# Kernel tuning notes

Measured on AMD Instinct MI355X. Metric: run time of the kernel, lower is better.

The kernel has to match this reference:

```python
import jax, jax.numpy as jnp
import numpy as np


def setup_inputs() -> dict:
    key = jax.random.key(0)
    ks = jax.random.split(key, 12)
    B, T, N, H = 32, 128, 256, 512
    s = 0.05
    return {
        "data": jax.random.normal(ks[0], (B, T, N), jnp.float32),
        "h0": jax.random.normal(ks[1], (B, H), jnp.float32),
        "gru_kernel": jax.random.normal(ks[2], (N, 3 * H), jnp.float32) * s,
        "gru_rkernel": jax.random.normal(ks[3], (H, 3 * H), jnp.float32) * s,
        "gru_bias": jax.random.normal(ks[4], (2, 3 * H), jnp.float32) * s,  # (input_bias, recurrent_bias), reset_after=True
        "w1_w": jax.random.normal(ks[5], (T, T), jnp.float32) * s,
        "w1_b": jax.random.normal(ks[6], (T,), jnp.float32) * s,
        "w2_w": jax.random.normal(ks[7], (H, T), jnp.float32) * s,
        "w2_b": jax.random.normal(ks[8], (T,), jnp.float32) * s,
        "v_w": jax.random.normal(ks[9], (T, 1), jnp.float32) * s,
        "v_b": jax.random.normal(ks[10], (1,), jnp.float32) * s,
        "n": N,
    }


def reference(data, h0, gru_kernel, gru_rkernel, gru_bias, w1_w, w1_b, w2_w, w2_b, v_w, v_b, n):
    B, T, N = data.shape
    b_in, b_rec = gru_bias[0], gru_bias[1]

    # Keras GRUCell (reset_after=True, gate order z,r,h)
    def step(h, x_t):
        mx = x_t @ gru_kernel + b_in          # (B,3H)
        mh = h @ gru_rkernel + b_rec          # (B,3H)
        xz, xr, xh = jnp.split(mx, 3, axis=-1)
        hz, hr, hh = jnp.split(mh, 3, axis=-1)
        z = jax.nn.sigmoid(xz + hz)
        r = jax.nn.sigmoid(xr + hr)
        c = jnp.tanh(xh + r * hh)
        h_new = z * h + (1.0 - z) * c
        return h_new, h_new

    xs = jnp.swapaxes(data, 0, 1)                               # (T,B,N)
    _, hs = jax.lax.scan(step, h0, xs)                          # (T,B,H) hidden state after each step

    # Input attention, vectorized over t (attention does not feed back into the GRU)
    x_perm = jnp.swapaxes(data, 1, 2)                           # (B,N,T)
    score_x = jnp.einsum('bnt,tu->bnu', x_perm, w1_w) + w1_b    # (B,N,T), constant across steps
    h_proj = hs @ w2_w + w2_b                                   # (T,B,T)
    e = jnp.tanh(score_x[None, :, :, :] + h_proj[:, :, None, :])  # (T,B,N,T)
    score = jnp.einsum('tbnu,u->tbn', e, v_w[:, 0]) + v_b[0]    # (T,B,N)
    alpha = jax.nn.softmax(score, axis=-1)                      # (T,B,N) softmax over features

    # Replicates tf.reshape(alpha_seq.stack(), (-1, T, n)) on (T,B,1,N) (row-major)
    alpha_seq = alpha.reshape(-1, T, N)                         # (B,T,N) via flat reindex, as in original
    return data * alpha_seq
```

## Files before the change

kernel.cpp:

```cpp
#include <hip/hip_runtime.h>
#include <math.h>

#define BB 32
#define TT 128
#define NF 256
#define HH 512
#define G3 1536
#define NWG 64

__device__ __forceinline__ float sigmoidf_(float x) { return 1.f / (1.f + __expf(-x)); }
__device__ __forceinline__ float tanh_fast(float x) {
    float e = __expf(2.f * x);
    return 1.f - 2.f / (e + 1.f);
}
__device__ __forceinline__ float sel4_(float a0, float a1, float a2, float a3, int s) {
    float s01 = (s & 1) ? a1 : a0;
    float s23 = (s & 1) ? a3 : a2;
    return (s & 2) ? s23 : s01;
}

__global__ __launch_bounds__(256) void k_hinit(const float* __restrict__ h0,
                                               float* __restrict__ hg2) {
    int idx = blockIdx.x * 256 + threadIdx.x;
    int i = idx & 511, b = idx >> 9;
    hg2[i * BB + b] = h0[b * HH + i];
}

__global__ __launch_bounds__(256) void k_pack(const float* __restrict__ rk,
                                              float4* __restrict__ rk4) {
    int gidx = blockIdx.x * 256 + threadIdx.x;
    int wg = gidx >> 12;
    int idx = gidx & 4095;
    int k = idx >> 3, s = idx & 7;
    int jjL = s ^ (((k >> 7) & 3) << 1);
    const float* r = rk + (size_t)k * G3 + wg * 8 + jjL;
    rk4[gidx] = make_float4(r[0], r[512], r[1024], 0.f);
}

__global__ __launch_bounds__(256) void k_mx(const float* __restrict__ data,
                                            const float* __restrict__ gk,
                                            const float* __restrict__ bias_in,
                                            float* __restrict__ mxT) {
    __shared__ __align__(16) float xs[NF * 8];
    int bx = blockIdx.x;
    int t = bx >> 2, b0 = (bx & 3) * 8;
    int tid = threadIdx.x;
    for (int idx = tid; idx < 8 * NF; idx += 256) {
        int bb = idx >> 8, k = idx & 255;
        xs[k * 8 + bb] = data[((size_t)(b0 + bb) * TT + t) * NF + k];
    }
    __syncthreads();
    float acc[6][8];
#pragma unroll
    for (int jj = 0; jj < 6; jj++)
#pragma unroll
        for (int bb = 0; bb < 8; bb++) acc[jj][bb] = 0.f;

    for (int k = 0; k < NF; k++) {
        float4 xa = *(const float4*)&xs[k * 8];
        float4 xb = *(const float4*)&xs[k * 8 + 4];
        float xv[8] = {xa.x, xa.y, xa.z, xa.w, xb.x, xb.y, xb.z, xb.w};
#pragma unroll
        for (int jj = 0; jj < 6; jj++) {
            float g = gk[(size_t)k * G3 + jj * 256 + tid];
#pragma unroll
            for (int bb = 0; bb < 8; bb++) acc[jj][bb] += g * xv[bb];
        }
    }
#pragma unroll
    for (int jj = 0; jj < 6; jj++) {
        int j = jj * 256 + tid;
        float bi = bias_in[j];
#pragma unroll
        for (int bb = 0; bb < 8; bb++)
            mxT[((size_t)t * G3 + j) * BB + b0 + bb] = acc[jj][bb] + bi;
    }
}

extern __shared__ float4 wl4_dyn[];

__global__ __launch_bounds__(256, 1) void k_gstep(const float4* __restrict__ rk4,
                                                  const float* __restrict__ gbias,
                                                  const float* __restrict__ mxT,
                                                  float* __restrict__ hg2,
                                                  float* __restrict__ hs,
                                                  int t) {
    __shared__ __align__(16) float4 h4[HH * 8];
    const int tid = threadIdx.x;
    const int wg  = blockIdx.x;
    const int jj  = tid >> 5;
    const int bq  = (tid >> 2) & 7;
    const int ks  = tid & 3;
    const int i0  = wg * 8;
    const int i   = i0 + jj;
    const int batch = bq * 4 + ks;
    const int jjs = jj ^ (ks << 1);
    const int bqs = bq ^ (ks << 1);

    {
        const float4* src = rk4 + (size_t)wg * 4096;
#pragma unroll
        for (int it = 0; it < 16; it++) {
            int idx = it * 256 + tid;
            wl4_dyn[idx] = src[idx];
        }
    }
    {
        const float4* hgr = (const float4*)(hg2 + (t & 1) * (HH * BB));
#pragma unroll
        for (int it = 0; it < 16; it++) {
            int idx = it * 256 + tid;
            h4[idx] = hgr[idx ^ ((((idx >> 10) & 3)) << 1)];
        }
    }
    const float* brec = gbias + G3;
    const float bz = brec[i], br_ = brec[512 + i], bh = brec[1024 + i];
    __syncthreads();

    const float* mxc = mxT + (size_t)t * G3 * BB;
    float mz = mxc[(size_t)i * BB + batch];
    float mr = mxc[(size_t)(512 + i) * BB + batch];
    float mh = mxc[(size_t)(1024 + i) * BB + batch];

    float az0 = 0.f, az1 = 0.f, az2 = 0.f, az3 = 0.f;
    float ar0 = 0.f, ar1 = 0.f, ar2 = 0.f, ar3 = 0.f;
    float ah0 = 0.f, ah1 = 0.f, ah2 = 0.f, ah3 = 0.f;
    const float4* wp  = wl4_dyn + ks * 1024 + jjs;
    const float4* hp2 = &h4[ks * 1024 + bqs];
#pragma unroll 4
    for (int kk = 0; kk < 128; kk++) {
        float4 w = wp[kk * 8];
        float4 h = hp2[kk * 8];
        az0 += w.x * h.x; az1 += w.x * h.y; az2 += w.x * h.z; az3 += w.x * h.w;
        ar0 += w.y * h.x; ar1 += w.y * h.y; ar2 += w.y * h.z; ar3 += w.y * h.w;
        ah0 += w.z * h.x; ah1 += w.z * h.y; ah2 += w.z * h.z; ah3 += w.z * h.w;
    }

    az0 += __shfl_xor(az0, 1); az1 += __shfl_xor(az1, 1);
    az2 += __shfl_xor(az2, 1); az3 += __shfl_xor(az3, 1);
    ar0 += __shfl_xor(ar0, 1); ar1 += __shfl_xor(ar1, 1);
    ar2 += __shfl_xor(ar2, 1); ar3 += __shfl_xor(ar3, 1);
    ah0 += __shfl_xor(ah0, 1); ah1 += __shfl_xor(ah1, 1);
    ah2 += __shfl_xor(ah2, 1); ah3 += __shfl_xor(ah3, 1);
    az0 += __shfl_xor(az0, 2); az1 += __shfl_xor(az1, 2);
    az2 += __shfl_xor(az2, 2); az3 += __shfl_xor(az3, 2);
    ar0 += __shfl_xor(ar0, 2); ar1 += __shfl_xor(ar1, 2);
    ar2 += __shfl_xor(ar2, 2); ar3 += __shfl_xor(ar3, 2);
    ah0 += __shfl_xor(ah0, 2); ah1 += __shfl_xor(ah1, 2);
    ah2 += __shfl_xor(ah2, 2); ah3 += __shfl_xor(ah3, 2);

    float azt = sel4_(az0, az1, az2, az3, ks);
    float art = sel4_(ar0, ar1, ar2, ar3, ks);
    float aht = sel4_(ah0, ah1, ah2, ah3, ks);

    float z = sigmoidf_(mz + azt + bz);
    float r = sigmoidf_(mr + art + br_);
    float c = tanhf(mh + r * (aht + bh));
    float hold = ((const float*)&h4[i * 8 + (bq ^ ((((i >> 7) & 3)) << 1))])[ks];
    float hn = z * hold + (1.f - z) * c;

    hg2[((t + 1) & 1) * (HH * BB) + i * BB + batch] = hn;

    __syncthreads();
    float* hstage = (float*)wl4_dyn;
    hstage[jj * 36 + batch] = hn;
    __syncthreads();
    {
        int b2 = tid >> 3, ii = tid & 7;
        hs[((size_t)t * BB + b2) * HH + i0 + ii] = hstage[ii * 36 + b2];
    }
}

__global__ __launch_bounds__(256) void k_sx(const float* __restrict__ data,
                                            const float* __restrict__ w1,
                                            const float* __restrict__ w1b,
                                            float* __restrict__ sx) {
    int bx = blockIdx.x;
    int b = bx >> 4, ug = bx & 15;
    int n = threadIdx.x;
    float acc[8] = {0, 0, 0, 0, 0, 0, 0, 0};
    const float* dp = data + (size_t)b * TT * NF + n;
    for (int t = 0; t < TT; t++) {
        float x = dp[(size_t)t * NF];
#pragma unroll
        for (int uu = 0; uu < 8; uu++) acc[uu] += x * w1[t * TT + ug * 8 + uu];
    }
#pragma unroll
    for (int uu = 0; uu < 8; uu++) {
        int u = ug * 8 + uu;
        sx[((size_t)b * TT + u) * NF + n] = acc[uu] + w1b[u];
    }
}

__global__ __launch_bounds__(256) void k_hp(const float* __restrict__ hs,
                                            const float* __restrict__ w2,
                                            const float* __restrict__ w2b,
                                            float* __restrict__ hp) {
    __shared__ float hsl[8 * HH];
    int r0 = blockIdx.x * 8;
    int tid = threadIdx.x;
    for (int idx = tid; idx < 8 * HH; idx += 256)
        hsl[idx] = hs[(size_t)r0 * HH + idx];
    __syncthreads();
    int u = tid & 127, rh = tid >> 7;
    float acc[4] = {0, 0, 0, 0};
    for (int k = 0; k < HH; k++) {
        float w = w2[k * TT + u];
#pragma unroll
        for (int rr = 0; rr < 4; rr++) acc[rr] += hsl[(rh * 4 + rr) * HH + k] * w;
    }
    float wb = w2b[u];
#pragma unroll
    for (int rr = 0; rr < 4; rr++)
        hp[(size_t)(r0 + rh * 4 + rr) * TT + u] = acc[rr] + wb;
}

__global__ __launch_bounds__(256) void k_attn(const float* __restrict__ data,
                                              const float* __restrict__ sx,
                                              const float* __restrict__ hp,
                                              const float* __restrict__ v_w,
                                              const float* __restrict__ v_b,
                                              float* __restrict__ out) {
    __shared__ float hv[TT];
    __shared__ float vv[TT];
    __shared__ float red[8];
    int r = blockIdx.x;
    int b = r & 31;
    int n = threadIdx.x;
    if (n < TT) {
        hv[n] = hp[(size_t)r * TT + n];
        vv[n] = v_w[n];
    }
    __syncthreads();
    float s = v_b[0];
    const float* sxp = sx + (size_t)b * TT * NF + n;
    for (int u = 0; u < TT; u++) {
        float e = tanh_fast(sxp[(size_t)u * NF] + hv[u]);
        s += vv[u] * e;
    }
    float m = s;
#pragma unroll
    for (int off = 32; off >= 1; off >>= 1) m = fmaxf(m, __shfl_xor(m, off));
    int lane = n & 63, wid = n >> 6;
    if (lane == 0) red[wid] = m;
    __syncthreads();
    float bm = fmaxf(fmaxf(red[0], red[1]), fmaxf(red[2], red[3]));
    float p = __expf(s - bm);
    float ps = p;
#pragma unroll
    for (int off = 32; off >= 1; off >>= 1) ps += __shfl_xor(ps, off);
    if (lane == 0) red[4 + wid] = ps;
    __syncthreads();
    float denom = red[4] + red[5] + red[6] + red[7];
    float alpha = p / denom;
    size_t idx = (size_t)r * NF + n;
    out[idx] = data[idx] * alpha;
}

extern "C" void kernel_launch(void* const* d_in, const int* in_sizes, int n_in,
                              void* d_out, int out_size, void* d_ws, size_t ws_size,
                              hipStream_t stream) {
    const float* data = (const float*)d_in[0];
    const float* h0   = (const float*)d_in[1];
    const float* gk   = (const float*)d_in[2];
    const float* rk   = (const float*)d_in[3];
    const float* gb   = (const float*)d_in[4];
    const float* w1   = (const float*)d_in[5];
    const float* w1b  = (const float*)d_in[6];
    const float* w2   = (const float*)d_in[7];
    const float* w2b  = (const float*)d_in[8];
    const float* vw   = (const float*)d_in[9];
    const float* vb   = (const float*)d_in[10];
    float* out = (float*)d_out;

    float* ws  = (float*)d_ws;
    float* mxT = ws;
    float* hs  = mxT + 6291456;
    float* sxb = hs + 2097152;
    float* hpb = sxb + 1048576;
    float* hg2 = hpb + 524288;
    float4* rk4 = (float4*)(hg2 + 32768);

    k_hinit<<<64, 256, 0, stream>>>(h0, hg2);
    k_pack<<<1024, 256, 0, stream>>>(rk, rk4);
    k_mx<<<512, 256, 0, stream>>>(data, gk, gb, mxT);

    for (int t = 0; t < TT; t++)
        k_gstep<<<NWG, 256, 65536, stream>>>(rk4, gb, mxT, hg2, hs, t);

    k_sx<<<512, 256, 0, stream>>>(data, w1, w1b, sxb);
    k_hp<<<512, 256, 0, stream>>>(hs, w2, w2b, hpb);
    k_attn<<<4096, 256, 0, stream>>>(data, sxb, hpb, vw, vb, out);
}
```

Baseline: 1.278 ms.

## Use direct global-to-LDS loads, merge init kernels, split k_mx wider

The per-step GRU kernel now stages recurrent weights and hidden state into shared memory with global_load_lds intrinsics, so the copies no longer pass through registers. The h-init and weight-pack kernels are merged into one launch, and k_mx is split three ways over gate columns to raise its workgroup count. tanh uses a hardware reciprocal and the attention loop is unrolled. Risks: the async LDS loads must complete before the barrier, and the fast reciprocal changes precision slightly.

After: 1.176 ms. 8.0% less time.

```diff
diff --git a/kernel.cpp b/kernel.cpp
--- a/kernel.cpp
+++ b/kernel.cpp
@@ -11,7 +11,7 @@
 __device__ __forceinline__ float sigmoidf_(float x) { return 1.f / (1.f + __expf(-x)); }
 __device__ __forceinline__ float tanh_fast(float x) {
     float e = __expf(2.f * x);
-    return 1.f - 2.f / (e + 1.f);
+    return 1.f - 2.f * __builtin_amdgcn_rcpf(e + 1.f);
 }
 __device__ __forceinline__ float sel4_(float a0, float a1, float a2, float a3, int s) {
     float s01 = (s & 1) ? a1 : a0;
@@ -19,22 +19,24 @@
     return (s & 2) ? s23 : s01;
 }
 
-__global__ __launch_bounds__(256) void k_hinit(const float* __restrict__ h0,
-                                               float* __restrict__ hg2) {
-    int idx = blockIdx.x * 256 + threadIdx.x;
-    int i = idx & 511, b = idx >> 9;
-    hg2[i * BB + b] = h0[b * HH + i];
-}
-
-__global__ __launch_bounds__(256) void k_pack(const float* __restrict__ rk,
-                                              float4* __restrict__ rk4) {
-    int gidx = blockIdx.x * 256 + threadIdx.x;
-    int wg = gidx >> 12;
-    int idx = gidx & 4095;
-    int k = idx >> 3, s = idx & 7;
-    int jjL = s ^ (((k >> 7) & 3) << 1);
-    const float* r = rk + (size_t)k * G3 + wg * 8 + jjL;
-    rk4[gidx] = make_float4(r[0], r[512], r[1024], 0.f);
+__global__ __launch_bounds__(256) void k_packinit(const float* __restrict__ rk,
+                                                  float4* __restrict__ rk4,
+                                                  const float* __restrict__ h0,
+                                                  float* __restrict__ hg2) {
+    int bid = blockIdx.x;
+    if (bid < 1024) {
+        int gidx = bid * 256 + threadIdx.x;
+        int wg = gidx >> 12;
+        int idx = gidx & 4095;
+        int k = idx >> 3, s = idx & 7;
+        int jjL = s ^ (((k >> 7) & 3) << 1);
+        const float* r = rk + (size_t)k * G3 + wg * 8 + jjL;
+        rk4[gidx] = make_float4(r[0], r[512], r[1024], 0.f);
+    } else {
+        int idx = (bid - 1024) * 256 + threadIdx.x;
+        int i = idx & 511, b = idx >> 9;
+        hg2[i * BB + b] = h0[b * HH + i];
+    }
 }
 
 __global__ __launch_bounds__(256) void k_mx(const float* __restrict__ data,
@@ -43,33 +45,38 @@
                                             float* __restrict__ mxT) {
     __shared__ __align__(16) float xs[NF * 8];
     int bx = blockIdx.x;
-    int t = bx >> 2, b0 = (bx & 3) * 8;
+    int t = bx / 12;
+    int rem = bx - t * 12;
+    int bg = rem / 3;
+    int jth = rem - bg * 3;
+    int b0 = bg * 8;
     int tid = threadIdx.x;
     for (int idx = tid; idx < 8 * NF; idx += 256) {
         int bb = idx >> 8, k = idx & 255;
         xs[k * 8 + bb] = data[((size_t)(b0 + bb) * TT + t) * NF + k];
     }
     __syncthreads();
-    float acc[6][8];
-#pragma unroll
-    for (int jj = 0; jj < 6; jj++)
+    float acc[2][8];
+#pragma unroll
+    for (int jj = 0; jj < 2; jj++)
 #pragma unroll
         for (int bb = 0; bb < 8; bb++) acc[jj][bb] = 0.f;
 
+    const float* gkc = gk + jth * 512 + tid;
     for (int k = 0; k < NF; k++) {
         float4 xa = *(const float4*)&xs[k * 8];
         float4 xb = *(const float4*)&xs[k * 8 + 4];
         float xv[8] = {xa.x, xa.y, xa.z, xa.w, xb.x, xb.y, xb.z, xb.w};
 #pragma unroll
-        for (int jj = 0; jj < 6; jj++) {
-            float g = gk[(size_t)k * G3 + jj * 256 + tid];
+        for (int jj = 0; jj < 2; jj++) {
+            float g = gkc[(size_t)k * G3 + jj * 256];
 #pragma unroll
             for (int bb = 0; bb < 8; bb++) acc[jj][bb] += g * xv[bb];
         }
     }
 #pragma unroll
-    for (int jj = 0; jj < 6; jj++) {
-        int j = jj * 256 + tid;
+    for (int jj = 0; jj < 2; jj++) {
+        int j = jth * 512 + jj * 256 + tid;
         float bi = bias_in[j];
 #pragma unroll
         for (int bb = 0; bb < 8; bb++)
@@ -102,7 +109,9 @@
 #pragma unroll
         for (int it = 0; it < 16; it++) {
             int idx = it * 256 + tid;
-            wl4_dyn[idx] = src[idx];
+            __builtin_amdgcn_global_load_lds(
+                (const __attribute__((address_space(1))) void*)(src + idx),
+                (__attribute__((address_space(3))) void*)&wl4_dyn[idx], 16, 0, 0);
         }
     }
     {
@@ -110,7 +119,10 @@
 #pragma unroll
         for (int it = 0; it < 16; it++) {
             int idx = it * 256 + tid;
-            h4[idx] = hgr[idx ^ ((((idx >> 10) & 3)) << 1)];
+            int sidx = idx ^ ((((idx >> 10) & 3)) << 1);
+            __builtin_amdgcn_global_load_lds(
+                (const __attribute__((address_space(1))) void*)(hgr + sidx),
+                (__attribute__((address_space(3))) void*)&h4[idx], 16, 0, 0);
         }
     }
     const float* brec = gbias + G3;
@@ -234,6 +246,7 @@
     __syncthreads();
     float s = v_b[0];
     const float* sxp = sx + (size_t)b * TT * NF + n;
+#pragma unroll 4
     for (int u = 0; u < TT; u++) {
         float e = tanh_fast(sxp[(size_t)u * NF] + hv[u]);
         s += vv[u] * e;
@@ -281,9 +294,8 @@
     float* hg2 = hpb + 524288;
     float4* rk4 = (float4*)(hg2 + 32768);
 
-    k_hinit<<<64, 256, 0, stream>>>(h0, hg2);
-    k_pack<<<1024, 256, 0, stream>>>(rk, rk4);
-    k_mx<<<512, 256, 0, stream>>>(data, gk, gb, mxT);
+    k_packinit<<<1088, 256, 0, stream>>>(rk, rk4, h0, hg2);
+    k_mx<<<1536, 256, 0, stream>>>(data, gk, gb, mxT);
 
     for (int t = 0; t < TT; t++)
         k_gstep<<<NWG, 256, 65536, stream>>>(rk4, gb, mxT, hg2, hs, t);
```
